# Performance work log

Measured on AMD Instinct MI355X. Metric: run time of the kernel, lower is better.

The kernel has to match this reference:

```python
import jax, jax.numpy as jnp
import numpy as np

EPS = 1e-5  # torch LayerNorm default
NUM_HEADS = 12


def layer_norm(x, g, b):
    m = jnp.mean(x, axis=-1, keepdims=True)
    v = jnp.var(x, axis=-1, keepdims=True)
    return (x - m) * jax.lax.rsqrt(v + EPS) * g + b


def split_heads(x):
    B, N, C = x.shape
    return x.reshape(B, N, NUM_HEADS, C // NUM_HEADS).transpose(0, 2, 1, 3)  # [B,H,N,D]


def merge_heads(x):
    B, H, N, D = x.shape
    return x.transpose(0, 2, 1, 3).reshape(B, N, H * D)


def attn_core(q, k, v, mask):
    # q:[B,H,Nq,D], k/v:[B,H,Nk,D], mask:[B,Nk] float (1=keep)
    d = q.shape[-1]
    scores = jnp.einsum('bhqd,bhkd->bhqk', q, k) * (d ** -0.5)
    scores = scores + (1.0 - mask)[:, None, None, :] * -5.0
    a = jax.nn.softmax(scores, axis=-1)
    return jnp.einsum('bhqk,bhkd->bhqd', a, v)


def setup_inputs() -> dict:
    key = jax.random.key(0)
    B, N, C = 4, 1024, 768
    Hd = C * 4  # mlp hidden = 3072
    ks = jax.random.split(key, 12)
    s = 0.02
    inp = {
        'x': jax.random.normal(ks[0], (B, N, C), jnp.float32),
        'encoder_out': jax.random.normal(ks[1], (B, N, C), jnp.float32),
        'mask': jnp.ones((B, N), jnp.float32),
        'encoder_mask': jnp.ones((B, N), jnp.float32),
        'ln1_g': jnp.ones((C,), jnp.float32), 'ln1_b': jnp.zeros((C,), jnp.float32),
        'qkv_w': jax.random.normal(ks[2], (C, 3 * C), jnp.float32) * s,
        'sa_proj_w': jax.random.normal(ks[3], (C, C), jnp.float32) * s,
        'sa_proj_b': jnp.zeros((C,), jnp.float32),
        'ln2_g': jnp.ones((C,), jnp.float32), 'ln2_b': jnp.zeros((C,), jnp.float32),
        'q_w': jax.random.normal(ks[4], (C, C), jnp.float32) * s,
        'kv_w': jax.random.normal(ks[5], (C, 2 * C), jnp.float32) * s,
        'ca_proj_w': jax.random.normal(ks[6], (C, C), jnp.float32) * s,
        'ca_proj_b': jnp.zeros((C,), jnp.float32),
        'ln3_g': jnp.ones((C,), jnp.float32), 'ln3_b': jnp.zeros((C,), jnp.float32),
        'fc1_w': jax.random.normal(ks[7], (C, Hd), jnp.float32) * s,
        'fc1_b': jnp.zeros((Hd,), jnp.float32),
        'fc2_w': jax.random.normal(ks[8], (Hd, C), jnp.float32) * s,
        'fc2_b': jnp.zeros((C,), jnp.float32),
    }
    return inp


def reference(x, encoder_out, mask, encoder_mask,
              ln1_g, ln1_b, qkv_w, sa_proj_w, sa_proj_b,
              ln2_g, ln2_b, q_w, kv_w, ca_proj_w, ca_proj_b,
              ln3_g, ln3_b, fc1_w, fc1_b, fc2_w, fc2_b):
    B, N, C = x.shape
    D = C // NUM_HEADS
    # --- self attention ---
    h = layer_norm(x, ln1_g, ln1_b)
    qkv = (h @ qkv_w).reshape(B, N, 3, NUM_HEADS, D)
    q = qkv[:, :, 0].transpose(0, 2, 1, 3)
    k = qkv[:, :, 1].transpose(0, 2, 1, 3)
    v = qkv[:, :, 2].transpose(0, 2, 1, 3)
    o = merge_heads(attn_core(q, k, v, mask)) @ sa_proj_w + sa_proj_b
    x = x + o
    # --- cross attention ---
    h = layer_norm(x, ln2_g, ln2_b)
    q = split_heads(h @ q_w)
    Be, Ne, Ce = encoder_out.shape
    kv = (encoder_out @ kv_w).reshape(Be, Ne, 2, NUM_HEADS, D)
    k = kv[:, :, 0].transpose(0, 2, 1, 3)
    v = kv[:, :, 1].transpose(0, 2, 1, 3)
    o = merge_heads(attn_core(q, k, v, encoder_mask)) @ ca_proj_w + ca_proj_b
    x = x + o
    # --- MLP (exact GELU, like torch nn.GELU default) ---
    h = layer_norm(x, ln3_g, ln3_b)
    h = jax.nn.gelu(h @ fc1_w + fc1_b, approximate=False) @ fc2_w + fc2_b
    return x + h
```

## Files before the change

### kernel.cpp

```cpp
#include <hip/hip_runtime.h>

typedef __attribute__((ext_vector_type(8))) __bf16 bf16x8;
typedef __attribute__((ext_vector_type(4))) float f32x4;

__device__ __forceinline__ void gload_lds16(const __bf16* g, __bf16* l) {
    __builtin_amdgcn_global_load_lds(
        (const __attribute__((address_space(1))) void*)g,
        (__attribute__((address_space(3))) void*)l,
        16, 0, 0);
}

template <int N> struct WaitVm;
#define WV(n) template <> struct WaitVm<n> { static __device__ __forceinline__ void run() { \
    asm volatile("s_waitcnt vmcnt(" #n ")" ::: "memory"); } };
WV(0) WV(3) WV(4) WV(6) WV(8) WV(9) WV(12)
#undef WV

__global__ void transpose_f2b(const float* __restrict__ in, __bf16* __restrict__ outp,
                              int R, int Ccols) {
    __shared__ __bf16 tile[32][33];
    int bx = blockIdx.x * 32, by = blockIdx.y * 32;
    int tx = threadIdx.x & 31, ty = threadIdx.x >> 5;
#pragma unroll
    for (int i = ty; i < 32; i += 8)
        tile[i][tx] = (__bf16)in[(size_t)(by + i) * Ccols + bx + tx];
    __syncthreads();
#pragma unroll
    for (int i = ty; i < 32; i += 8)
        outp[(size_t)(bx + i) * R + by + tx] = tile[tx][i];
}

__global__ void cvt_f2b(const float* __restrict__ in, __bf16* __restrict__ outp) {
    int i = blockIdx.x * blockDim.x + threadIdx.x;
    float4 v = ((const float4*)in)[i];
    __bf16 o4[4] = {(__bf16)v.x, (__bf16)v.y, (__bf16)v.z, (__bf16)v.w};
    *(uint2*)(outp + (size_t)i * 4) = *(const uint2*)o4;
}

__global__ __launch_bounds__(256) void ln_kernel(const float* __restrict__ x,
                                                 const float* __restrict__ g,
                                                 const float* __restrict__ b,
                                                 __bf16* __restrict__ o) {
    int row = blockIdx.x, tid = threadIdx.x;
    const float* xr = x + (size_t)row * 768;
    float v0 = xr[tid], v1 = xr[tid + 256], v2 = xr[tid + 512];
    float s = v0 + v1 + v2, s2 = v0 * v0 + v1 * v1 + v2 * v2;
#pragma unroll
    for (int d = 32; d >= 1; d >>= 1) {
        s += __shfl_xor(s, d);
        s2 += __shfl_xor(s2, d);
    }
    __shared__ float red[8];
    int wave = tid >> 6, lane = tid & 63;
    if (!lane) { red[wave] = s; red[4 + wave] = s2; }
    __syncthreads();
    s = red[0] + red[1] + red[2] + red[3];
    s2 = red[4] + red[5] + red[6] + red[7];
    float mean = s * (1.0f / 768.0f);
    float var = s2 * (1.0f / 768.0f) - mean * mean;
    float inv = rsqrtf(var + 1e-5f);
    o[(size_t)row * 768 + tid]       = (__bf16)((v0 - mean) * inv * g[tid]       + b[tid]);
    o[(size_t)row * 768 + tid + 256] = (__bf16)((v1 - mean) * inv * g[tid + 256] + b[tid + 256]);
    o[(size_t)row * 768 + tid + 512] = (__bf16)((v2 - mean) * inv * g[tid + 512] + b[tid + 512]);
}

template <int BM, int NS, int BIAS, int RESID, int GELU, typename TO>
__global__ __launch_bounds__(256, 2) void gemm_nt(
    const __bf16* __restrict__ A, int lda,
    const __bf16* __restrict__ Bt, int ldb,
    TO* __restrict__ C, int ldc,
    const float* __restrict__ bias,
    const float* __restrict__ resid,
    int K) {
    __shared__ __bf16 lA[NS][BM * 32];
    __shared__ __bf16 lB[NS][128 * 32];
    constexpr int L = (BM == 128) ? 4 : 3;
    constexpr int WCOLS = 256 / BM;
    constexpr int NF = (BM == 128) ? 4 : 2;
    constexpr int WNSP = (BM == 128) ? 64 : 32;
    const int tid = threadIdx.x;
    const int wave = tid >> 6, lane = tid & 63;
    const int wm = wave / WCOLS, wn = wave % WCOLS;
    const int bn = blockIdx.x * 128, bm = blockIdx.y * BM;
    const int ln15 = lane & 15, hi = lane >> 4;

    f32x4 acc[4][NF] = {};

    const int srow = tid >> 2;
    const int scol = (((tid & 3) ^ ((srow >> 1) & 3)) * 8);
    const __bf16* gA0 = A + (size_t)(bm + srow) * lda + scol;
    const __bf16* gA1 = A + (size_t)(bm + 64 + srow) * lda + scol;
    const __bf16* gB0 = Bt + (size_t)(bn + srow) * ldb + scol;
    const __bf16* gB1 = Bt + (size_t)(bn + 64 + srow) * ldb + scol;

    const int rswz = (hi * 8) ^ (((ln15 >> 1) & 3) * 8);
    const int rAoff = (wm * 64 + ln15) * 32 + rswz;
    const int rBoff = (wn * WNSP + ln15) * 32 + rswz;

    auto STAGE = [&](int buf, int k0) {
        gload_lds16(gA0 + k0, lA[buf] + wave * 512);
        if constexpr (BM == 128) gload_lds16(gA1 + k0, lA[buf] + 2048 + wave * 512);
        gload_lds16(gB0 + k0, lB[buf] + wave * 512);
        gload_lds16(gB1 + k0, lB[buf] + 2048 + wave * 512);
    };
    auto COMPUTE = [&](int buf) {
        const __bf16* rA = lA[buf] + rAoff;
        const __bf16* rB = lB[buf] + rBoff;
        bf16x8 af[4], bfr[NF];
#pragma unroll
        for (int m = 0; m < 4; ++m) af[m] = *(const bf16x8*)(rA + m * 512);
#pragma unroll
        for (int n = 0; n < NF; ++n) bfr[n] = *(const bf16x8*)(rB + n * 512);
#pragma unroll
        for (int m = 0; m < 4; ++m)
#pragma unroll
            for (int n = 0; n < NF; ++n)
                acc[m][n] = __builtin_amdgcn_mfma_f32_16x16x32_bf16(af[m], bfr[n], acc[m][n], 0, 0, 0);
    };
    auto inc = [](int b) { return (b + 1 == NS) ? 0 : b + 1; };

    const int nt = K >> 5;
#pragma unroll
    for (int s = 0; s < NS - 1; ++s) STAGE(s, s << 5);
    int sbuf = NS - 1, cbuf = 0;
    for (int t = 0; t <= nt - NS; ++t) {
        STAGE(sbuf, (t + NS - 1) << 5);
        sbuf = inc(sbuf);
        WaitVm<(NS - 1) * L>::run();
        __builtin_amdgcn_s_barrier();
        __builtin_amdgcn_sched_barrier(0);
        COMPUTE(cbuf);
        cbuf = inc(cbuf);
        __builtin_amdgcn_sched_barrier(0);
        __builtin_amdgcn_s_barrier();
    }
    if constexpr (NS >= 4) {
        WaitVm<2 * L>::run();
        __builtin_amdgcn_s_barrier();
        __builtin_amdgcn_sched_barrier(0);
        COMPUTE(cbuf); cbuf = inc(cbuf);
        __builtin_amdgcn_sched_barrier(0);
        __builtin_amdgcn_s_barrier();
    }
    if constexpr (NS >= 3) {
        WaitVm<L>::run();
        __builtin_amdgcn_s_barrier();
        __builtin_amdgcn_sched_barrier(0);
        COMPUTE(cbuf); cbuf = inc(cbuf);
        __builtin_amdgcn_sched_barrier(0);
        __builtin_amdgcn_s_barrier();
    }
    WaitVm<0>::run();
    __builtin_amdgcn_s_barrier();
    __builtin_amdgcn_sched_barrier(0);
    COMPUTE(cbuf);

#pragma unroll
    for (int m = 0; m < 4; ++m)
#pragma unroll
        for (int n = 0; n < NF; ++n)
#pragma unroll
            for (int r = 0; r < 4; ++r) {
                int row = bm + wm * 64 + m * 16 + hi * 4 + r;
                int col = bn + wn * WNSP + n * 16 + ln15;
                float v = acc[m][n][r];
                if (BIAS) v += bias[col];
                if (GELU) v = 0.5f * v * (1.0f + erff(v * 0.70710678118f));
                if (RESID) v += resid[(size_t)row * ldc + col];
                C[(size_t)row * ldc + col] = (TO)v;
            }
}

__global__ __launch_bounds__(256, 2) void attn_kernel(
    const __bf16* __restrict__ Qp, int ldq, int qcol,
    const __bf16* __restrict__ Kp, int ldk, int kcol,
    const __bf16* __restrict__ Vp, int ldv, int vcol,
    const float* __restrict__ mask,
    __bf16* __restrict__ Out) {
    __shared__ __bf16 lK[64 * 64];
    __shared__ __bf16 lV[64 * 64];
    __shared__ __bf16 lP[4][16 * 64];
    const int tid = threadIdx.x, wave = tid >> 6, lane = tid & 63;
    const int bh = blockIdx.y, b = bh / 12, h = bh % 12;
    const int qt = blockIdx.x;
    const int ln15 = lane & 15, hi = lane >> 4;

    const __bf16* qrow = Qp + (size_t)(b * 1024 + qt * 64 + wave * 16 + ln15) * ldq + qcol + h * 64;
    bf16x8 qf0 = *(const bf16x8*)(qrow + hi * 8);
    bf16x8 qf1 = *(const bf16x8*)(qrow + 32 + hi * 8);

    float l_part[4] = {0.f, 0.f, 0.f, 0.f};
    f32x4 oacc[4] = {};

    const int skey = tid >> 3;
    const int ssrc = (((tid & 7) ^ (skey & 7)) * 8);
    const __bf16* gK = Kp + (size_t)(b * 1024 + skey) * ldk + kcol + h * 64 + ssrc;
    __bf16* lK0 = lK + wave * 512;
    __bf16* lK1 = lK + 2048 + wave * 512;

    const int vkey = tid & 63;
    const int vdb = wave * 16;
    const __bf16* gV = Vp + (size_t)(b * 1024 + vkey) * ldv + vcol + h * 64 + vdb;

    const int kswz = (lane & 7) * 8;
    const __bf16* rK = lK + ln15 * 64;
    const __bf16* rV = lV + ln15 * 64;
    __bf16* wP = lP[wave];
    const __bf16* rP = lP[wave] + ln15 * 64;

    const float C1 = 0.18033688f;
    for (int kt = 0; kt < 16; ++kt) {
        const size_t tb = (size_t)kt * 64;
        gload_lds16(gK + tb * ldk, lK0);
        gload_lds16(gK + (tb + 32) * ldk, lK1);
        bf16x8 v0 = *(const bf16x8*)(gV + tb * ldv);
        bf16x8 v1 = *(const bf16x8*)(gV + tb * ldv + 8);
#pragma unroll
        for (int j = 0; j < 8; ++j) {
            lV[(vdb + j) * 64 + (vkey ^ (j * 8))] = v0[j];
            lV[(vdb + 8 + j) * 64 + (vkey ^ (j * 8))] = v1[j];
        }
        __syncthreads();

        f32x4 s[4];
#pragma unroll
        for (int n = 0; n < 4; ++n) {
            bf16x8 kf0 = *(const bf16x8*)(rK + n * 1024 + ((hi * 8) ^ kswz));
            bf16x8 kf1 = *(const bf16x8*)(rK + n * 1024 + ((hi * 8 + 32) ^ kswz));
            f32x4 z = {};
            z = __builtin_amdgcn_mfma_f32_16x16x32_bf16(qf0, kf0, z, 0, 0, 0);
            s[n] = __builtin_amdgcn_mfma_f32_16x16x32_bf16(qf1, kf1, z, 0, 0, 0);
        }
        float mb2[4];
#pragma unroll
        for (int n = 0; n < 4; ++n)
            mb2[n] = (1.0f - mask[b * 1024 + kt * 64 + n * 16 + ln15]) * -7.2134752f;

#pragma unroll
        for (int n = 0; n < 4; ++n)
#pragma unroll
            for (int r = 0; r < 4; ++r) {
                s[n][r] = exp2f(s[n][r] * C1 + mb2[n]);
                l_part[r] += s[n][r];
            }

#pragma unroll
        for (int n = 0; n < 4; ++n)
#pragma unroll
            for (int r = 0; r < 4; ++r) {
                int prow = hi * 4 + r;
                wP[prow * 64 + ((n * 16 + ln15) ^ ((prow & 7) * 8))] = (__bf16)s[n][r];
            }
        bf16x8 pf0 = *(const bf16x8*)(rP + ((hi * 8) ^ kswz));
        bf16x8 pf1 = *(const bf16x8*)(rP + ((hi * 8 + 32) ^ kswz));
#pragma unroll
        for (int n = 0; n < 4; ++n) {
            bf16x8 vf0 = *(const bf16x8*)(rV + n * 1024 + ((hi * 8) ^ kswz));
            bf16x8 vf1 = *(const bf16x8*)(rV + n * 1024 + ((hi * 8 + 32) ^ kswz));
            oacc[n] = __builtin_amdgcn_mfma_f32_16x16x32_bf16(pf0, vf0, oacc[n], 0, 0, 0);
            oacc[n] = __builtin_amdgcn_mfma_f32_16x16x32_bf16(pf1, vf1, oacc[n], 0, 0, 0);
        }
        __syncthreads();
    }

#pragma unroll
    for (int r = 0; r < 4; ++r) {
#pragma unroll
        for (int d = 1; d < 16; d <<= 1) l_part[r] += __shfl_xor(l_part[r], d);
        l_part[r] = 1.0f / l_part[r];
    }

#pragma unroll
    for (int n = 0; n < 4; ++n)
#pragma unroll
        for (int r = 0; r < 4; ++r) {
            int row = b * 1024 + qt * 64 + wave * 16 + hi * 4 + r;
            int col = h * 64 + n * 16 + ln15;
            Out[(size_t)row * 768 + col] = (__bf16)(oacc[n][r] * l_part[r]);
        }
}

extern "C" void kernel_launch(void* const* d_in, const int* in_sizes, int n_in,
                              void* d_out, int out_size, void* d_ws, size_t ws_size,
                              hipStream_t stream) {
    const float* x     = (const float*)d_in[0];
    const float* enc   = (const float*)d_in[1];
    const float* mask  = (const float*)d_in[2];
    const float* emask = (const float*)d_in[3];
    const float* ln1_g = (const float*)d_in[4];
    const float* ln1_b = (const float*)d_in[5];
    const float* qkv_w = (const float*)d_in[6];
    const float* sa_w  = (const float*)d_in[7];
    const float* sa_b  = (const float*)d_in[8];
    const float* ln2_g = (const float*)d_in[9];
    const float* ln2_b = (const float*)d_in[10];
    const float* q_w   = (const float*)d_in[11];
    const float* kv_w  = (const float*)d_in[12];
    const float* ca_w  = (const float*)d_in[13];
    const float* ca_b  = (const float*)d_in[14];
    const float* ln3_g = (const float*)d_in[15];
    const float* ln3_b = (const float*)d_in[16];
    const float* fc1_w = (const float*)d_in[17];
    const float* fc1_b = (const float*)d_in[18];
    const float* fc2_w = (const float*)d_in[19];
    const float* fc2_b = (const float*)d_in[20];
    float* out = (float*)d_out;

    char* w = (char*)d_ws;
    size_t off = 0;
    auto alloc = [&](size_t bytes) { void* p = w + off; off += bytes; return p; };
    __bf16* qkv_t = (__bf16*)alloc((size_t)2304 * 768 * 2);
    __bf16* sa_t  = (__bf16*)alloc((size_t)768 * 768 * 2);
    __bf16* q_t   = (__bf16*)alloc((size_t)768 * 768 * 2);
    __bf16* kv_t  = (__bf16*)alloc((size_t)1536 * 768 * 2);
    __bf16* ca_t  = (__bf16*)alloc((size_t)768 * 768 * 2);
    __bf16* fc1_t = (__bf16*)alloc((size_t)3072 * 768 * 2);
    __bf16* fc2_t = (__bf16*)alloc((size_t)768 * 3072 * 2);
    __bf16* H     = (__bf16*)alloc((size_t)4096 * 768 * 2);
    __bf16* QKV   = (__bf16*)alloc((size_t)4096 * 2304 * 2);
    __bf16* ATT   = (__bf16*)alloc((size_t)4096 * 768 * 2);
    float*  X1    = (float*)alloc((size_t)4096 * 768 * 4);
    float*  X2    = (float*)alloc((size_t)4096 * 768 * 4);
    __bf16* encb  = (__bf16*)alloc((size_t)4096 * 768 * 2);
    __bf16* HID   = QKV;
    __bf16* Qb    = QKV;
    __bf16* KVb   = QKV + (size_t)4096 * 768;

    dim3 blk(256);
    transpose_f2b<<<dim3(72, 24), blk, 0, stream>>>(qkv_w, qkv_t, 768, 2304);
    transpose_f2b<<<dim3(24, 24), blk, 0, stream>>>(sa_w, sa_t, 768, 768);
    transpose_f2b<<<dim3(24, 24), blk, 0, stream>>>(q_w, q_t, 768, 768);
    transpose_f2b<<<dim3(48, 24), blk, 0, stream>>>(kv_w, kv_t, 768, 1536);
    transpose_f2b<<<dim3(24, 24), blk, 0, stream>>>(ca_w, ca_t, 768, 768);
    transpose_f2b<<<dim3(96, 24), blk, 0, stream>>>(fc1_w, fc1_t, 768, 3072);
    transpose_f2b<<<dim3(24, 96), blk, 0, stream>>>(fc2_w, fc2_t, 3072, 768);
    cvt_f2b<<<dim3(3072), blk, 0, stream>>>(enc, encb);

    ln_kernel<<<4096, blk, 0, stream>>>(x, ln1_g, ln1_b, H);
    gemm_nt<128, 3, 0, 0, 0, __bf16><<<dim3(18, 32), blk, 0, stream>>>(H, 768, qkv_t, 768, QKV, 2304, nullptr, nullptr, 768);
    attn_kernel<<<dim3(16, 48), blk, 0, stream>>>(QKV, 2304, 0, QKV, 2304, 768, QKV, 2304, 1536, mask, ATT);
    gemm_nt<64, 4, 1, 1, 0, float><<<dim3(6, 64), blk, 0, stream>>>(ATT, 768, sa_t, 768, X1, 768, sa_b, x, 768);
    ln_kernel<<<4096, blk, 0, stream>>>(X1, ln2_g, ln2_b, H);
    gemm_nt<64, 4, 0, 0, 0, __bf16><<<dim3(6, 64), blk, 0, stream>>>(H, 768, q_t, 768, Qb, 768, nullptr, nullptr, 768);
    gemm_nt<128, 3, 0, 0, 0, __bf16><<<dim3(12, 32), blk, 0, stream>>>(encb, 768, kv_t, 768, KVb, 1536, nullptr, nullptr, 768);
    attn_kernel<<<dim3(16, 48), blk, 0, stream>>>(Qb, 768, 0, KVb, 1536, 0, KVb, 1536, 768, emask, ATT);
    gemm_nt<64, 4, 1, 1, 0, float><<<dim3(6, 64), blk, 0, stream>>>(ATT, 768, ca_t, 768, X2, 768, ca_b, X1, 768);
    ln_kernel<<<4096, blk, 0, stream>>>(X2, ln3_g, ln3_b, H);
    gemm_nt<128, 3, 1, 0, 1, __bf16><<<dim3(24, 32), blk, 0, stream>>>(H, 768, fc1_t, 768, HID, 3072, fc1_b, nullptr, 768);
    gemm_nt<64, 4, 1, 1, 0, float><<<dim3(6, 64), blk, 0, stream>>>(HID, 3072, fc2_t, 3072, out, 768, fc2_b, X2, 3072);
}
```

Baseline: 432.3 us.

## Split-K the fc2 GEMM and remap workgroup ids across XCDs

The fc2 GEMM (K=3072) is split into two K halves that write fp32 partials, and a separate reduction kernel then adds bias and residual. The GEMM and attention kernels also remap linear workgroup ids so that neighbouring tiles land on the same XCD, which should improve L2 reuse. The split-K path doubles the number of fc2 workgroups to fill more CUs, at the cost of an extra 25 MB partial buffer round trip and one more kernel launch.

```diff
diff --git a/kernel.cpp b/kernel.cpp
--- a/kernel.cpp
+++ b/kernel.cpp
@@ -64,7 +64,36 @@
     o[(size_t)row * 768 + tid + 512] = (__bf16)((v2 - mean) * inv * g[tid + 512] + b[tid + 512]);
 }
 
-template <int BM, int NS, int BIAS, int RESID, int GELU, typename TO>
+template <int BIAS, int RESID, int GELU, typename TO>
+__global__ __launch_bounds__(256) void reduce_splitk(
+    const float* __restrict__ P, TO* __restrict__ C,
+    const float* __restrict__ bias, const float* __restrict__ resid,
+    int total4, int ncols) {
+    int i = blockIdx.x * 256 + threadIdx.x;
+    if (i >= total4) return;
+    float4 a = ((const float4*)P)[i];
+    float4 b = ((const float4*)P)[i + total4];
+    float v[4] = {a.x + b.x, a.y + b.y, a.z + b.z, a.w + b.w};
+    int col = (i * 4) % ncols;
+    if (BIAS) {
+        float4 bs = *(const float4*)(bias + col);
+        v[0] += bs.x; v[1] += bs.y; v[2] += bs.z; v[3] += bs.w;
+    }
+    if (GELU)
+#pragma unroll
+        for (int j = 0; j < 4; ++j) v[j] = 0.5f * v[j] * (1.0f + erff(v[j] * 0.70710678118f));
+    if (RESID) {
+        float4 r = ((const float4*)resid)[i];
+        v[0] += r.x; v[1] += r.y; v[2] += r.z; v[3] += r.w;
+    }
+    TO o4[4] = {(TO)v[0], (TO)v[1], (TO)v[2], (TO)v[3]};
+    *(TO*)(&((TO*)C)[(size_t)i * 4]) = o4[0];
+    ((TO*)C)[(size_t)i * 4 + 1] = o4[1];
+    ((TO*)C)[(size_t)i * 4 + 2] = o4[2];
+    ((TO*)C)[(size_t)i * 4 + 3] = o4[3];
+}
+
+template <int BM, int NS, int SPLITK, int BIAS, int RESID, int GELU, typename TO>
 __global__ __launch_bounds__(256, 2) void gemm_nt(
     const __bf16* __restrict__ A, int lda,
     const __bf16* __restrict__ Bt, int ldb,
@@ -81,8 +110,20 @@
     const int tid = threadIdx.x;
     const int wave = tid >> 6, lane = tid & 63;
     const int wm = wave / WCOLS, wn = wave % WCOLS;
-    const int bn = blockIdx.x * 128, bm = blockIdx.y * BM;
     const int ln15 = lane & 15, hi = lane >> 4;
+
+    const int lin = blockIdx.x + blockIdx.y * gridDim.x;
+    const int nwg = gridDim.x * gridDim.y;
+    const int t0 = (lin & 7) * (nwg >> 3) + (lin >> 3);
+    const int bn = (t0 % gridDim.x) * 128, bm = (t0 / gridDim.x) * BM;
+
+    if constexpr (SPLITK > 1) {
+        const int kz = blockIdx.z;
+        K /= SPLITK;
+        A += (size_t)kz * K;
+        Bt += (size_t)kz * K;
+        C += (size_t)kz * 4096 * ldc;
+    }
 
     f32x4 acc[4][NF] = {};
 
@@ -181,8 +222,10 @@
     __shared__ __bf16 lV[64 * 64];
     __shared__ __bf16 lP[4][16 * 64];
     const int tid = threadIdx.x, wave = tid >> 6, lane = tid & 63;
-    const int bh = blockIdx.y, b = bh / 12, h = bh % 12;
-    const int qt = blockIdx.x;
+    const int lin = blockIdx.x + blockIdx.y * 16;
+    const int t0 = (lin & 7) * 96 + (lin >> 3);
+    const int qt = t0 & 15, bh = t0 >> 4;
+    const int b = bh / 12, h = bh % 12;
     const int ln15 = lane & 15, hi = lane >> 4;
 
     const __bf16* qrow = Qp + (size_t)(b * 1024 + qt * 64 + wave * 16 + ln15) * ldq + qcol + h * 64;
@@ -322,6 +365,7 @@
     float*  X1    = (float*)alloc((size_t)4096 * 768 * 4);
     float*  X2    = (float*)alloc((size_t)4096 * 768 * 4);
     __bf16* encb  = (__bf16*)alloc((size_t)4096 * 768 * 2);
+    float*  PK    = (float*)alloc((size_t)2 * 4096 * 768 * 4);
     __bf16* HID   = QKV;
     __bf16* Qb    = QKV;
     __bf16* KVb   = QKV + (size_t)4096 * 768;
@@ -337,15 +381,16 @@
     cvt_f2b<<<dim3(3072), blk, 0, stream>>>(enc, encb);
 
     ln_kernel<<<4096, blk, 0, stream>>>(x, ln1_g, ln1_b, H);
-    gemm_nt<128, 3, 0, 0, 0, __bf16><<<dim3(18, 32), blk, 0, stream>>>(H, 768, qkv_t, 768, QKV, 2304, nullptr, nullptr, 768);
+    gemm_nt<128, 3, 1, 0, 0, 0, __bf16><<<dim3(18, 32), blk, 0, stream>>>(H, 768, qkv_t, 768, QKV, 2304, nullptr, nullptr, 768);
     attn_kernel<<<dim3(16, 48), blk, 0, stream>>>(QKV, 2304, 0, QKV, 2304, 768, QKV, 2304, 1536, mask, ATT);
-    gemm_nt<64, 4, 1, 1, 0, float><<<dim3(6, 64), blk, 0, stream>>>(ATT, 768, sa_t, 768, X1, 768, sa_b, x, 768);
+    gemm_nt<64, 4, 1, 1, 1, 0, float><<<dim3(6, 64), blk, 0, stream>>>(ATT, 768, sa_t, 768, X1, 768, sa_b, x, 768);
     ln_kernel<<<4096, blk, 0, stream>>>(X1, ln2_g, ln2_b, H);
-    gemm_nt<64, 4, 0, 0, 0, __bf16><<<dim3(6, 64), blk, 0, stream>>>(H, 768, q_t, 768, Qb, 768, nullptr, nullptr, 768);
-    gemm_nt<128, 3, 0, 0, 0, __bf16><<<dim3(12, 32), blk, 0, stream>>>(encb, 768, kv_t, 768, KVb, 1536, nullptr, nullptr, 768);
+    gemm_nt<64, 4, 1, 0, 0, 0, __bf16><<<dim3(6, 64), blk, 0, stream>>>(H, 768, q_t, 768, Qb, 768, nullptr, nullptr, 768);
+    gemm_nt<128, 3, 1, 0, 0, 0, __bf16><<<dim3(12, 32), blk, 0, stream>>>(encb, 768, kv_t, 768, KVb, 1536, nullptr, nullptr, 768);
     attn_kernel<<<dim3(16, 48), blk, 0, stream>>>(Qb, 768, 0, KVb, 1536, 0, KVb, 1536, 768, emask, ATT);
-    gemm_nt<64, 4, 1, 1, 0, float><<<dim3(6, 64), blk, 0, stream>>>(ATT, 768, ca_t, 768, X2, 768, ca_b, X1, 768);
+    gemm_nt<64, 4, 1, 1, 1, 0, float><<<dim3(6, 64), blk, 0, stream>>>(ATT, 768, ca_t, 768, X2, 768, ca_b, X1, 768);
     ln_kernel<<<4096, blk, 0, stream>>>(X2, ln3_g, ln3_b, H);
-    gemm_nt<128, 3, 1, 0, 1, __bf16><<<dim3(24, 32), blk, 0, stream>>>(H, 768, fc1_t, 768, HID, 3072, fc1_b, nullptr, 768);
-    gemm_nt<64, 4, 1, 1, 0, float><<<dim3(6, 64), blk, 0, stream>>>(HID, 3072, fc2_t, 3072, out, 768, fc2_b, X2, 3072);
-}
+    gemm_nt<128, 3, 1, 1, 0, 1, __bf16><<<dim3(24, 32), blk, 0, stream>>>(H, 768, fc1_t, 768, HID, 3072, fc1_b, nullptr, 768);
+    gemm_nt<64, 4, 2, 0, 0, 0, float><<<dim3(6, 64, 2), blk, 0, stream>>>(HID, 3072, fc2_t, 3072, PK, 768, nullptr, nullptr, 3072);
+    reduce_splitk<1, 1, 0, float><<<dim3(3072), blk, 0, stream>>>(PK, out, fc2_b, X2, 786432, 768);
+}
```

Result: faster. 418.7 us (-3.2%).
